# Kernel tuning notes

Hardware: AMD Instinct MI355X
Metric: run time of the kernel (lower is better)

## Reference

```python
import jax, jax.numpy as jnp
import numpy as np

B, S, D = 8, 1024, 1024
H, DK = 16, 64  # num_heads, d_k; H*DK == D
NEG_INF = 1e29


def setup_inputs() -> dict:
    key = jax.random.key(0)
    ks = jax.random.split(key, 12)
    sc = 1.0 / np.sqrt(D)
    q = jax.random.normal(ks[0], (B, S, D), jnp.float32)
    k = jax.random.normal(ks[1], (B, S, D), jnp.float32)
    v = jax.random.normal(ks[2], (B, S, D), jnp.float32)
    # causal mask, broadcast per batch (mask==0 positions are masked out)
    mask = jnp.broadcast_to(jnp.tril(jnp.ones((S, S), jnp.int32)), (B, S, S))
    Wq = jax.random.normal(ks[3], (D, D), jnp.float32) * sc
    bq = jax.random.normal(ks[4], (D,), jnp.float32) * 0.01
    Wk = jax.random.normal(ks[5], (D, D), jnp.float32) * sc
    bk = jax.random.normal(ks[6], (D,), jnp.float32) * 0.01
    Wv = jax.random.normal(ks[7], (D, D), jnp.float32) * sc
    bv = jax.random.normal(ks[8], (D,), jnp.float32) * 0.01
    Wo = jax.random.normal(ks[9], (D, D), jnp.float32) * sc
    bo = jax.random.normal(ks[10], (D,), jnp.float32) * 0.01
    return {"q": q, "k": k, "v": v, "mask": mask,
            "Wq": Wq, "bq": bq, "Wk": Wk, "bk": bk,
            "Wv": Wv, "bv": bv, "Wo": Wo, "bo": bo}


def reference(q, k, v, mask, Wq, bq, Wk, bk, Wv, bv, Wo, bo):
    # Linear projections (torch Linear: x @ W.T + b)
    q1 = q @ Wq.T + bq
    k1 = k @ Wk.T + bk
    v1 = v @ Wv.T + bv
    # [B, S, D] -> [B, H, S, DK]
    def split_heads(x):
        return x.reshape(B, S, H, DK).transpose(0, 2, 1, 3)
    q3, k3, v3 = split_heads(q1), split_heads(k1), split_heads(v1)
    # scores [B, H, S, S]
    scores = jnp.einsum('bhqd,bhkd->bhqk', q3, k3) / jnp.sqrt(jnp.float32(DK))
    scores = jnp.where(mask[:, None, :, :] == 0, -NEG_INF, scores)
    probs = jax.nn.softmax(scores, axis=-1)
    attn = jnp.einsum('bhqk,bhkd->bhqd', probs, v3)  # [B, H, S, DK]
    out = attn.transpose(0, 2, 1, 3).reshape(B, S, D)
    return out @ Wo.T + bo
```

## Files before the change

### kernel.cpp

```cpp
#include <hip/hip_runtime.h>
#include <hip/hip_bf16.h>
#include <stdint.h>

constexpr int NB = 8;
constexpr int NS = 1024;
constexpr int ND = 1024;
constexpr int NH = 16;
constexpr int NDK = 64;
constexpr int NT = NS / 64;

typedef __bf16 bf16_t;
typedef __attribute__((ext_vector_type(8))) __bf16 bf16x8;
typedef __attribute__((ext_vector_type(4))) __bf16 bf16x4;
typedef __attribute__((ext_vector_type(4))) float f32x4;

#define GLL16(g, s) __builtin_amdgcn_global_load_lds( \
    (const __attribute__((address_space(1))) void*)(g), \
    (__attribute__((address_space(3))) void*)(s), 16, 0, 0)

__device__ __forceinline__ void cvt_body(const float* __restrict__ s,
                                         bf16_t* __restrict__ d, long n) {
  long i0 = (long)(blockIdx.x * blockDim.x + threadIdx.x) * 4;
  long step = (long)gridDim.x * blockDim.x * 4;
  for (long i = i0; i < n; i += step) {
    float4 f = *(const float4*)(s + i);
    bf16x4 o;
    o[0] = (bf16_t)f.x; o[1] = (bf16_t)f.y; o[2] = (bf16_t)f.z; o[3] = (bf16_t)f.w;
    *(bf16x4*)(d + i) = o;
  }
}

__global__ __launch_bounds__(256) void cvt3_kernel(const float* s0, bf16_t* d0,
                                                   const float* s1, bf16_t* d1,
                                                   const float* s2, bf16_t* d2, long n) {
  const float* s = blockIdx.y == 0 ? s0 : blockIdx.y == 1 ? s1 : s2;
  bf16_t* d = blockIdx.y == 0 ? d0 : blockIdx.y == 1 ? d1 : d2;
  cvt_body(s, d, n);
}

__global__ __launch_bounds__(256) void cvt4_kernel(const float* s0, bf16_t* d0,
                                                   const float* s1, bf16_t* d1,
                                                   const float* s2, bf16_t* d2,
                                                   const float* s3, bf16_t* d3, long n) {
  const float* s = blockIdx.y == 0 ? s0 : blockIdx.y == 1 ? s1 : blockIdx.y == 2 ? s2 : s3;
  bf16_t* d = blockIdx.y == 0 ? d0 : blockIdx.y == 1 ? d1 : blockIdx.y == 2 ? d2 : d3;
  cvt_body(s, d, n);
}

template<bool OUT_F32>
__device__ __forceinline__ void gemm_body(bf16_t* S,
                                          const bf16_t* __restrict__ A,
                                          const bf16_t* __restrict__ W,
                                          const float* __restrict__ bias,
                                          void* __restrict__ Cout,
                                          int M, int N, int K, int bx, int by) {
  const int tid = threadIdx.x;
  const int l = tid & 63, w = tid >> 6;
  const int wr = w >> 2, wc = w & 3;
  const int g = l >> 4, r = l & 15;
  const int m0 = by * 256, n0 = bx * 128;
  const int wbase = (tid & 448) * 8;

  auto stage = [&](int q, int t) {
    const int k0 = t << 6;
    bf16_t* As = S + q * 24576;
    bf16_t* Bs = As + 16384;
#pragma unroll
    for (int it = 0; it < 4; ++it) {
      int idx = it * 512 + tid;
      int row = idx >> 3, c = (idx & 7) ^ (row & 7);
      GLL16(A + (size_t)(m0 + row) * K + k0 + c * 8, As + it * 4096 + wbase);
    }
#pragma unroll
    for (int it = 0; it < 2; ++it) {
      int idx = it * 512 + tid;
      int row = idx >> 3, c = (idx & 7) ^ (row & 7);
      GLL16(W + (size_t)(n0 + row) * K + k0 + c * 8, Bs + it * 4096 + wbase);
    }
  };

  f32x4 acc[8][2] = {};
  const int NKT = K >> 6;

  stage(0, 0);
  stage(1, 1);

  int q = 0;
  for (int t = 0; t < NKT; ++t) {
    if (t + 2 < NKT) {
      int qn = q + 2; if (qn >= 3) qn -= 3;
      stage(qn, t + 2);
      asm volatile("s_waitcnt vmcnt(12)" ::: "memory");
    } else if (t + 1 < NKT) {
      asm volatile("s_waitcnt vmcnt(6)" ::: "memory");
    } else {
      asm volatile("s_waitcnt vmcnt(0)" ::: "memory");
    }
    __builtin_amdgcn_s_barrier();

    const bf16_t* a_ = S + q * 24576;
    const bf16_t* b_ = a_ + 16384;
#pragma unroll
    for (int kk = 0; kk < 2; ++kk) {
      bf16x8 af[8], bw[2];
#pragma unroll
      for (int m = 0; m < 8; ++m) {
        int row = wr * 128 + m * 16 + r;
        af[m] = *(const bf16x8*)(a_ + row * 64 + (((kk * 4 + g) ^ (row & 7)) << 3));
      }
#pragma unroll
      for (int n = 0; n < 2; ++n) {
        int row = wc * 32 + n * 16 + r;
        bw[n] = *(const bf16x8*)(b_ + row * 64 + (((kk * 4 + g) ^ (row & 7)) << 3));
      }
#pragma unroll
      for (int m = 0; m < 8; ++m)
#pragma unroll
        for (int n = 0; n < 2; ++n)
          acc[m][n] = __builtin_amdgcn_mfma_f32_16x16x32_bf16(af[m], bw[n], acc[m][n], 0, 0, 0);
    }
    asm volatile("s_waitcnt lgkmcnt(0)" ::: "memory");
    __builtin_amdgcn_s_barrier();
    ++q; if (q >= 3) q -= 3;
  }

#pragma unroll
  for (int n = 0; n < 2; ++n) {
    int col = n0 + wc * 32 + n * 16 + r;
    float bv = bias[col];
#pragma unroll
    for (int m = 0; m < 8; ++m) {
      int row0 = m0 + wr * 128 + m * 16 + g * 4;
#pragma unroll
      for (int j = 0; j < 4; ++j) {
        float vv = acc[m][n][j] + bv;
        if (OUT_F32)
          ((float*)Cout)[(size_t)(row0 + j) * N + col] = vv;
        else
          ((bf16_t*)Cout)[(size_t)(row0 + j) * N + col] = (bf16_t)vv;
      }
    }
  }
}

__global__ __launch_bounds__(512, 2) void gemm_bt(const bf16_t* __restrict__ A,
                                                  const bf16_t* __restrict__ W,
                                                  const float* __restrict__ bias,
                                                  float* __restrict__ Cout,
                                                  int M, int N, int K) {
  __shared__ bf16_t S[3 * 24576];
  const int o = blockIdx.x;
  const int xcd = o & 7, s = o >> 3;
  const int bx = s & 7, u = s >> 3;
  const int by = xcd + 8 * u;
  gemm_body<true>(S, A, W, bias, (void*)Cout, M, N, K, bx, by);
}

__global__ __launch_bounds__(512, 2) void gemm_qkv(
    const bf16_t* A0, const bf16_t* W0, const float* b0, bf16_t* C0,
    const bf16_t* A1, const bf16_t* W1, const float* b1, bf16_t* C1,
    const bf16_t* A2, const bf16_t* W2, const float* b2, bf16_t* C2,
    int M, int N, int K) {
  __shared__ bf16_t S[3 * 24576];
  const int o = blockIdx.x;
  const int xcd = o & 7, s = o >> 3;
  const int bx = s & 7, u = s >> 3;
  const int zby = xcd + 8 * u;
  const int z = zby >> 5, by = zby & 31;
  const bf16_t* A = z == 0 ? A0 : z == 1 ? A1 : A2;
  const bf16_t* W = z == 0 ? W0 : z == 1 ? W1 : W2;
  const float* bb = z == 0 ? b0 : z == 1 ? b1 : b2;
  bf16_t* C = z == 0 ? C0 : z == 1 ? C1 : C2;
  gemm_body<false>(S, A, W, bb, (void*)C, M, N, K, bx, by);
}

__global__ __launch_bounds__(256, 4) void attn_kernel(const bf16_t* __restrict__ Q1,
                                                      const bf16_t* __restrict__ K1,
                                                      const bf16_t* __restrict__ V1,
                                                      bf16_t* __restrict__ attn) {
  __shared__ bf16_t Kt[2][64 * 64];
  __shared__ bf16_t Vt[2][64 * 64];
  __shared__ bf16_t Pl[4][16 * 64];

  const int tid = threadIdx.x;
  const int l = tid & 63, w = tid >> 6;
  const int g = l >> 4, r = l & 15;

  const int o = blockIdx.x;
  const int os = (o & 7) * 128 + (o >> 3);
  const int pair = os & 7, hb = os >> 3;
  const int h = hb & 15, b = hb >> 4;

  constexpr float SC = 0.18033688011112042f;

  for (int ph = 0; ph < 2; ++ph) {
    const int qt = ph ? (NT - 1 - pair) : pair;
    const int qrow_g = qt * 64 + w * 16 + r;

    const bf16_t* qptr = Q1 + ((size_t)b * NS + qrow_g) * ND + h * 64;
    bf16x8 qf0 = *(const bf16x8*)(qptr + g * 8);
    bf16x8 qf1 = *(const bf16x8*)(qptr + 32 + g * 8);
#pragma unroll
    for (int i = 0; i < 8; ++i) {
      qf0[i] = (bf16_t)((float)qf0[i] * SC);
      qf1[i] = (bf16_t)((float)qf1[i] * SC);
    }

    float mrun = -1e30f, lrun = 0.f;
    f32x4 oacc[4] = {};

    __syncthreads();

    bf16x8 vr0, vr1;
    {
#pragma unroll
      for (int it = 0; it < 2; ++it) {
        int idx = it * 256 + tid;
        int key = idx >> 3;
        int dkg = ((idx & 7) ^ (key & 7)) << 3;
        GLL16(K1 + ((size_t)b * NS + key) * ND + h * 64 + dkg,
              &Kt[0][(it * 256 + w * 64) * 8]);
      }
      vr0 = *(const bf16x8*)(V1 + ((size_t)b * NS + l) * ND + h * 64 + w * 8);
      vr1 = *(const bf16x8*)(V1 + ((size_t)b * NS + l) * ND + h * 64 + (4 + w) * 8);
    }

    for (int kt = 0; kt <= qt; ++kt) {
      const int p = kt & 1;
      const int k0 = kt * 64;

#pragma unroll
      for (int it = 0; it < 2; ++it) {
        int dkb = (it * 4 + w) * 8;
#pragma unroll
        for (int jj = 0; jj < 8; ++jj) {
          int dk = dkb + jj;
          int boff = dk * 128 + ((l * 2) ^ ((dk & 7) << 4));
          *(bf16_t*)((char*)Vt[p] + boff) = (it ? vr1 : vr0)[jj];
        }
      }
      __syncthreads();

      if (kt < qt) {
        const int k0n = k0 + 64;
#pragma unroll
        for (int it = 0; it < 2; ++it) {
          int idx = it * 256 + tid;
          int key = idx >> 3;
          int dkg = ((idx & 7) ^ (key & 7)) << 3;
          GLL16(K1 + ((size_t)b * NS + k0n + key) * ND + h * 64 + dkg,
                &Kt[p ^ 1][(it * 256 + w * 64) * 8]);
        }
        vr0 = *(const bf16x8*)(V1 + ((size_t)b * NS + k0n + l) * ND + h * 64 + w * 8);
        vr1 = *(const bf16x8*)(V1 + ((size_t)b * NS + k0n + l) * ND + h * 64 + (4 + w) * 8);
      }

      f32x4 sacc[4] = {};
      __builtin_amdgcn_s_setprio(1);
#pragma unroll
      for (int n = 0; n < 4; ++n) {
        int key = n * 16 + r;
#pragma unroll
        for (int kk = 0; kk < 2; ++kk) {
          int dk2 = kk * 32 + g * 8;
          int boff = key * 128 + ((dk2 * 2) ^ ((key & 7) << 4));
          bf16x8 kf = *(const bf16x8*)((char*)Kt[p] + boff);
          sacc[n] = __builtin_amdgcn_mfma_f32_16x16x32_bf16(kf, kk == 0 ? qf0 : qf1, sacc[n], 0, 0, 0);
        }
      }
      __builtin_amdgcn_s_setprio(0);

      if (kt == qt) {
#pragma unroll
        for (int n = 0; n < 4; ++n)
#pragma unroll
          for (int j = 0; j < 4; ++j)
            if (k0 + n * 16 + g * 4 + j > qrow_g) sacc[n][j] = -1e30f;
      }

      float mx;
      {
        float t0 = fmaxf(fmaxf(sacc[0][0], sacc[0][1]), fmaxf(sacc[0][2], sacc[0][3]));
        float t1 = fmaxf(fmaxf(sacc[1][0], sacc[1][1]), fmaxf(sacc[1][2], sacc[1][3]));
        float t2 = fmaxf(fmaxf(sacc[2][0], sacc[2][1]), fmaxf(sacc[2][2], sacc[2][3]));
        float t3 = fmaxf(fmaxf(sacc[3][0], sacc[3][1]), fmaxf(sacc[3][2], sacc[3][3]));
        mx = fmaxf(fmaxf(t0, t1), fmaxf(t2, t3));
      }
      mx = fmaxf(mx, __shfl_xor(mx, 16));
      mx = fmaxf(mx, __shfl_xor(mx, 32));

      if (!__all(mx <= mrun + 8.0f)) {
        float m_new = fmaxf(mrun, mx);
        float esc = __builtin_amdgcn_exp2f(mrun - m_new);
        mrun = m_new;
        lrun *= esc;
#pragma unroll
        for (int n = 0; n < 4; ++n)
#pragma unroll
          for (int j = 0; j < 4; ++j) oacc[n][j] *= esc;
      }

      float rsum = 0.f;
#pragma unroll
      for (int n = 0; n < 4; ++n) {
        bf16x4 p4;
#pragma unroll
        for (int j = 0; j < 4; ++j) {
          float pe = __builtin_amdgcn_exp2f(sacc[n][j] - mrun);
          rsum += pe;
          p4[j] = (bf16_t)pe;
        }
        *(bf16x4*)((char*)Pl[w] + r * 128 + ((n * 32 + g * 8) ^ ((r & 7) << 4))) = p4;
      }
      rsum += __shfl_xor(rsum, 16);
      rsum += __shfl_xor(rsum, 32);
      lrun += rsum;

      __builtin_amdgcn_s_setprio(1);
#pragma unroll
      for (int kk = 0; kk < 2; ++kk) {
        bf16x8 pf = *(const bf16x8*)((char*)Pl[w] + r * 128 + ((kk * 64 + g * 16) ^ ((r & 7) << 4)));
#pragma unroll
        for (int n = 0; n < 4; ++n) {
          int dkr = n * 16 + r;
          bf16x8 vf = *(const bf16x8*)((char*)Vt[p] + dkr * 128 + ((kk * 64 + g * 16) ^ ((r & 7) << 4)));
          oacc[n] = __builtin_amdgcn_mfma_f32_16x16x32_bf16(vf, pf, oacc[n], 0, 0, 0);
        }
      }
      __builtin_amdgcn_s_setprio(0);
    }

    float linv = 1.0f / lrun;
#pragma unroll
    for (int n = 0; n < 4; ++n) {
      bf16x4 o4;
#pragma unroll
      for (int j = 0; j < 4; ++j) o4[j] = (bf16_t)(oacc[n][j] * linv);
      *(bf16x4*)(attn + ((size_t)b * NS + qrow_g) * ND + h * 64 + n * 16 + g * 4) = o4;
    }
  }
}

extern "C" void kernel_launch(void* const* d_in, const int* in_sizes, int n_in,
                              void* d_out, int out_size, void* d_ws, size_t ws_size,
                              hipStream_t stream) {
  const float* q  = (const float*)d_in[0];
  const float* k  = (const float*)d_in[1];
  const float* v  = (const float*)d_in[2];
  const float* Wq = (const float*)d_in[4];
  const float* bq = (const float*)d_in[5];
  const float* Wk = (const float*)d_in[6];
  const float* bk = (const float*)d_in[7];
  const float* Wv = (const float*)d_in[8];
  const float* bv = (const float*)d_in[9];
  const float* Wo = (const float*)d_in[10];
  const float* bo = (const float*)d_in[11];
  float* out = (float*)d_out;

  const size_t NX = (size_t)NB * NS * ND;
  const size_t NW = (size_t)ND * ND;
  char* ws = (char*)d_ws;
  size_t off = 0;
  auto alloc = [&](size_t bytes) {
    char* p = ws + off;
    off += (bytes + 255) & ~(size_t)255;
    return p;
  };
  bf16_t* xq  = (bf16_t*)alloc(NX * 2);
  bf16_t* xk  = (bf16_t*)alloc(NX * 2);
  bf16_t* xv  = (bf16_t*)alloc(NX * 2);
  bf16_t* wqb = (bf16_t*)alloc(NW * 2);
  bf16_t* wkb = (bf16_t*)alloc(NW * 2);
  bf16_t* wvb = (bf16_t*)alloc(NW * 2);
  bf16_t* wob = (bf16_t*)alloc(NW * 2);
  bf16_t* q1  = (bf16_t*)alloc(NX * 2);
  bf16_t* k1  = (bf16_t*)alloc(NX * 2);
  bf16_t* v1  = (bf16_t*)alloc(NX * 2);
  bf16_t* at  = xq;

  dim3 blk(256);
  cvt3_kernel<<<dim3(1024, 3), blk, 0, stream>>>(q, xq, k, xk, v, xv, (long)NX);
  cvt4_kernel<<<dim3(128, 4), blk, 0, stream>>>(Wq, wqb, Wk, wkb, Wv, wvb, Wo, wob, (long)NW);

  gemm_qkv<<<dim3(768), dim3(512), 0, stream>>>(
      xq, wqb, bq, q1, xk, wkb, bk, k1, xv, wvb, bv, v1, NB * NS, ND, ND);

  attn_kernel<<<dim3((NT / 2) * NH * NB), blk, 0, stream>>>(q1, k1, v1, at);

  gemm_bt<<<dim3(256), dim3(512), 0, stream>>>(at, wob, bo, out, NB * NS, ND, ND);
}
```

Before: 157.0 us.

## Reshape GEMM warp tiling to 4x2 and interleave prefetch with MFMA phases

```diff
diff --git a/kernel.cpp b/kernel.cpp
--- a/kernel.cpp
+++ b/kernel.cpp
@@ -56,81 +56,85 @@
                                           int M, int N, int K, int bx, int by) {
   const int tid = threadIdx.x;
   const int l = tid & 63, w = tid >> 6;
-  const int wr = w >> 2, wc = w & 3;
+  const int wr = w >> 1, wc = w & 1;
   const int g = l >> 4, r = l & 15;
   const int m0 = by * 256, n0 = bx * 128;
-  const int wbase = (tid & 448) * 8;
-
-  auto stage = [&](int q, int t) {
-    const int k0 = t << 6;
-    bf16_t* As = S + q * 24576;
-    bf16_t* Bs = As + 16384;
-#pragma unroll
-    for (int it = 0; it < 4; ++it) {
-      int idx = it * 512 + tid;
-      int row = idx >> 3, c = (idx & 7) ^ (row & 7);
-      GLL16(A + (size_t)(m0 + row) * K + k0 + c * 8, As + it * 4096 + wbase);
-    }
-#pragma unroll
-    for (int it = 0; it < 2; ++it) {
-      int idx = it * 512 + tid;
-      int row = idx >> 3, c = (idx & 7) ^ (row & 7);
-      GLL16(W + (size_t)(n0 + row) * K + k0 + c * 8, Bs + it * 4096 + wbase);
-    }
+  const int wbase = w * 512;
+
+  auto stageA = [&](int q, int t, int it) {
+    int idx = it * 512 + tid;
+    int row = idx >> 3, c = (idx & 7) ^ (row & 7);
+    GLL16(A + (size_t)(m0 + row) * K + (t << 6) + c * 8,
+          S + q * 24576 + it * 4096 + wbase);
   };
-
-  f32x4 acc[8][2] = {};
+  auto stageB = [&](int q, int t, int it) {
+    int idx = it * 512 + tid;
+    int row = idx >> 3, c = (idx & 7) ^ (row & 7);
+    GLL16(W + (size_t)(n0 + row) * K + (t << 6) + c * 8,
+          S + q * 24576 + 16384 + it * 4096 + wbase);
+  };
+
+  f32x4 acc[4][4] = {};
   const int NKT = K >> 6;
 
-  stage(0, 0);
-  stage(1, 1);
+#pragma unroll
+  for (int it = 0; it < 4; ++it) stageA(0, 0, it);
+#pragma unroll
+  for (int it = 0; it < 2; ++it) stageB(0, 0, it);
+#pragma unroll
+  for (int it = 0; it < 4; ++it) stageA(1, 1, it);
+#pragma unroll
+  for (int it = 0; it < 2; ++it) stageB(1, 1, it);
 
   int q = 0;
   for (int t = 0; t < NKT; ++t) {
-    if (t + 2 < NKT) {
-      int qn = q + 2; if (qn >= 3) qn -= 3;
-      stage(qn, t + 2);
-      asm volatile("s_waitcnt vmcnt(12)" ::: "memory");
-    } else if (t + 1 < NKT) {
-      asm volatile("s_waitcnt vmcnt(6)" ::: "memory");
-    } else {
-      asm volatile("s_waitcnt vmcnt(0)" ::: "memory");
-    }
+    const bool pf = (t + 2 < NKT);
+    int q2 = q + 2; if (q2 >= 3) q2 -= 3;
+
+    if (t + 1 < NKT) asm volatile("s_waitcnt vmcnt(6)" ::: "memory");
+    else             asm volatile("s_waitcnt vmcnt(0)" ::: "memory");
     __builtin_amdgcn_s_barrier();
 
     const bf16_t* a_ = S + q * 24576;
     const bf16_t* b_ = a_ + 16384;
+
 #pragma unroll
     for (int kk = 0; kk < 2; ++kk) {
-      bf16x8 af[8], bw[2];
-#pragma unroll
-      for (int m = 0; m < 8; ++m) {
-        int row = wr * 128 + m * 16 + r;
+      bf16x8 af[4], bw[4];
+#pragma unroll
+      for (int m = 0; m < 4; ++m) {
+        int row = wr * 64 + m * 16 + r;
         af[m] = *(const bf16x8*)(a_ + row * 64 + (((kk * 4 + g) ^ (row & 7)) << 3));
       }
 #pragma unroll
-      for (int n = 0; n < 2; ++n) {
-        int row = wc * 32 + n * 16 + r;
+      for (int n = 0; n < 4; ++n) {
+        int row = wc * 64 + n * 16 + r;
         bw[n] = *(const bf16x8*)(b_ + row * 64 + (((kk * 4 + g) ^ (row & 7)) << 3));
       }
-#pragma unroll
-      for (int m = 0; m < 8; ++m)
-#pragma unroll
-        for (int n = 0; n < 2; ++n)
+      if (pf) {
+        if (kk == 0) { stageA(q2, t + 2, 0); stageA(q2, t + 2, 1); stageA(q2, t + 2, 2); }
+        else         { stageA(q2, t + 2, 3); stageB(q2, t + 2, 0); stageB(q2, t + 2, 1); }
+      }
+      __builtin_amdgcn_s_barrier();
+      __builtin_amdgcn_s_setprio(1);
+#pragma unroll
+      for (int m = 0; m < 4; ++m)
+#pragma unroll
+        for (int n = 0; n < 4; ++n)
           acc[m][n] = __builtin_amdgcn_mfma_f32_16x16x32_bf16(af[m], bw[n], acc[m][n], 0, 0, 0);
-    }
-    asm volatile("s_waitcnt lgkmcnt(0)" ::: "memory");
-    __builtin_amdgcn_s_barrier();
+      __builtin_amdgcn_s_setprio(0);
+      if (kk == 0) __builtin_amdgcn_s_barrier();
+    }
     ++q; if (q >= 3) q -= 3;
   }
 
 #pragma unroll
-  for (int n = 0; n < 2; ++n) {
-    int col = n0 + wc * 32 + n * 16 + r;
+  for (int n = 0; n < 4; ++n) {
+    int col = n0 + wc * 64 + n * 16 + r;
     float bv = bias[col];
 #pragma unroll
-    for (int m = 0; m < 8; ++m) {
-      int row0 = m0 + wr * 128 + m * 16 + g * 4;
+    for (int m = 0; m < 4; ++m) {
+      int row0 = m0 + wr * 64 + m * 16 + g * 4;
 #pragma unroll
       for (int j = 0; j < 4; ++j) {
         float vv = acc[m][n][j] + bv;
```

Measured after the change: 157.2 us. Within noise of the previous version (+0.1%).
